# Optimization experiments

Measured on AMD Instinct MI355X. Metric: run time of the kernel, lower is better.

## Reference

```python
import jax, jax.numpy as jnp
import numpy as np

DIM = 1024
HEADS = 16
WIN = 128          # local window size
BATCH = 4
SEQ = 4096
HEAD_DIM = DIM // HEADS
HIDDEN = 2 * DIM   # GEGLU hidden_dim = 2*dim
EPS = 1e-5
NEG_INF = -1e9


def layer_norm(x, g, b):
    m = jnp.mean(x, axis=-1, keepdims=True)
    v = jnp.mean((x - m) ** 2, axis=-1, keepdims=True)
    return (x - m) * jax.lax.rsqrt(v + EPS) * g + b


def sliding_causal_local_attn(x, wq, wk, wv, wo, bo, rel_bias):
    # x: [B, S, D]; sliding-window causal attention: each query attends to
    # its own window plus the previous window (look_backward=1), causally masked.
    B, S, D = x.shape
    h, w, dh = HEADS, WIN, HEAD_DIM
    nw = S // w
    scale = dh ** -0.5

    def split_heads(t):  # [B,S,D] -> [B,h,nw,w,dh]
        return t.reshape(B, S, h, dh).transpose(0, 2, 1, 3).reshape(B, h, nw, w, dh)

    q = split_heads(x @ wq)
    k = split_heads(x @ wk)
    v = split_heads(x @ wv)

    # context = [previous window ; current window] -> [B,h,nw,2w,dh]
    k_pad = jnp.pad(k, ((0, 0), (0, 0), (1, 0), (0, 0), (0, 0)))
    v_pad = jnp.pad(v, ((0, 0), (0, 0), (1, 0), (0, 0), (0, 0)))
    kc = jnp.concatenate([k_pad[:, :, :-1], k_pad[:, :, 1:]], axis=3)
    vc = jnp.concatenate([v_pad[:, :, :-1], v_pad[:, :, 1:]], axis=3)

    logits = jnp.einsum('bhnid,bhnjd->bhnij', q, kc) * scale  # [B,h,nw,w,2w]

    i = jnp.arange(w)[:, None]        # query pos within window
    j = jnp.arange(2 * w)[None, :]    # key pos within [prev;cur] context
    dist = i + w - j                  # relative distance, 0..2w-1 when causal
    causal = dist >= 0
    # learned relative position bias per head, indexed by distance
    bias = rel_bias[:, jnp.clip(dist, 0, 2 * w - 1)]  # [h, w, 2w]
    logits = logits + bias[None, :, None]

    n_idx = jnp.arange(nw)[:, None, None]
    valid = causal[None] & ((n_idx > 0) | (j[None] >= w))  # mask padded first window
    logits = jnp.where(valid[None, None], logits, NEG_INF)

    attn = jax.nn.softmax(logits, axis=-1)
    out = jnp.einsum('bhnij,bhnjd->bhnid', attn, vc)           # [B,h,nw,w,dh]
    out = out.reshape(B, h, S, dh).transpose(0, 2, 1, 3).reshape(B, S, D)
    return out @ wo + bo


def geglu(x, w1, b1, w2, b2):
    proj = x @ w1 + b1                         # [B,S,2*HIDDEN]
    val, gate = jnp.split(proj, 2, axis=-1)
    return (val * jax.nn.gelu(gate, approximate=False)) @ w2 + b2


def setup_inputs() -> dict:
    key = jax.random.key(0)
    ks = jax.random.split(key, 12)
    sd = 0.02
    return {
        'x': jax.random.normal(ks[0], (BATCH, SEQ, DIM), jnp.float32),
        'ln1_g': jnp.ones((DIM,), jnp.float32),
        'ln1_b': jnp.zeros((DIM,), jnp.float32),
        'ln2_g': jnp.ones((DIM,), jnp.float32),
        'ln2_b': jnp.zeros((DIM,), jnp.float32),
        'wq': jax.random.normal(ks[1], (DIM, DIM), jnp.float32) * sd,
        'wk': jax.random.normal(ks[2], (DIM, DIM), jnp.float32) * sd,
        'wv': jax.random.normal(ks[3], (DIM, DIM), jnp.float32) * sd,
        'wo': jax.random.normal(ks[4], (DIM, DIM), jnp.float32) * sd,
        'bo': jnp.zeros((DIM,), jnp.float32),
        'rel_bias': jax.random.normal(ks[5], (HEADS, 2 * WIN), jnp.float32) * sd,
        'w_ff1': jax.random.normal(ks[6], (DIM, 2 * HIDDEN), jnp.float32) * sd,
        'b_ff1': jnp.zeros((2 * HIDDEN,), jnp.float32),
        'w_ff2': jax.random.normal(ks[7], (HIDDEN, DIM), jnp.float32) * sd,
        'b_ff2': jnp.zeros((DIM,), jnp.float32),
    }


def reference(x, ln1_g, ln1_b, ln2_g, ln2_b, wq, wk, wv, wo, bo, rel_bias,
              w_ff1, b_ff1, w_ff2, b_ff2):
    x = x + sliding_causal_local_attn(layer_norm(x, ln1_g, ln1_b),
                                      wq, wk, wv, wo, bo, rel_bias)
    x = x + geglu(layer_norm(x, ln2_g, ln2_b), w_ff1, b_ff1, w_ff2, b_ff2)
    return x
```

## Files before the change

kernel.cpp:

```cpp
#include <hip/hip_runtime.h>
#include <math.h>

typedef __attribute__((ext_vector_type(8))) short s16x8;
typedef __attribute__((ext_vector_type(4))) float f32x4;

__device__ __forceinline__ float b2f(unsigned short u){
  unsigned int i = ((unsigned int)u) << 16;
  float f; __builtin_memcpy(&f, &i, 4); return f;
}
__device__ __forceinline__ unsigned short f2b(float f){
  unsigned int i; __builtin_memcpy(&i, &f, 4);
  unsigned int r = (i + 0x7fffu + ((i >> 16) & 1u)) >> 16;
  return (unsigned short)r;
}
__device__ __forceinline__ f32x4 mfma16(s16x8 a, s16x8 b, f32x4 c){
  return __builtin_amdgcn_mfma_f32_16x16x32_bf16(a, b, c, 0, 0, 0);
}
__device__ __forceinline__ float gelu_exact(float x){
  return 0.5f * x * (1.0f + erff(x * 0.70710678118654752f));
}
__device__ __forceinline__ void gl_lds16(const unsigned short* g, unsigned short* l){
  __builtin_amdgcn_global_load_lds(
      (const __attribute__((address_space(1))) unsigned int*)g,
      (__attribute__((address_space(3))) unsigned int*)l, 16, 0, 0);
}

__global__ void transpose_k(const float* __restrict__ in,
                            unsigned short* __restrict__ out, int R, int C){
  __shared__ unsigned short tile[32][33];
  int c0 = blockIdx.x * 32, r0 = blockIdx.y * 32;
  int tx = threadIdx.x, ty = threadIdx.y;
  #pragma unroll
  for(int i = 0; i < 4; i++)
    tile[ty + 8*i][tx] = f2b(in[(size_t)(r0 + ty + 8*i) * C + c0 + tx]);
  __syncthreads();
  #pragma unroll
  for(int i = 0; i < 4; i++)
    out[(size_t)(c0 + ty + 8*i) * R + r0 + tx] = tile[tx][ty + 8*i];
}

__global__ __launch_bounds__(256) void ln_k(const float* __restrict__ x,
                                            const float* __restrict__ g,
                                            const float* __restrict__ b,
                                            unsigned short* __restrict__ out){
  int row = blockIdx.x, t = threadIdx.x;
  const float4* xr = (const float4*)(x + (size_t)row * 1024);
  float4 u = xr[t];
  float s  = u.x + u.y + u.z + u.w;
  float ss = u.x*u.x + u.y*u.y + u.z*u.z + u.w*u.w;
  for(int o = 32; o; o >>= 1){ s += __shfl_down(s, o, 64); ss += __shfl_down(ss, o, 64); }
  __shared__ float red[16];
  int lane = t & 63, wv = t >> 6;
  if(!lane){ red[wv] = s; red[8 + wv] = ss; }
  __syncthreads();
  if(!t){
    float S  = red[0] + red[1] + red[2] + red[3];
    float SS = red[8] + red[9] + red[10] + red[11];
    float m  = S * (1.0f/1024.0f);
    float var = SS * (1.0f/1024.0f) - m*m;
    red[0] = m; red[1] = rsqrtf(var + 1e-5f);
  }
  __syncthreads();
  float m = red[0], inv = red[1];
  float4 ug = ((const float4*)g)[t];
  float4 ub = ((const float4*)b)[t];
  ushort4 o4;
  o4.x = f2b((u.x - m) * inv * ug.x + ub.x);
  o4.y = f2b((u.y - m) * inv * ug.y + ub.y);
  o4.z = f2b((u.z - m) * inv * ug.z + ub.z);
  o4.w = f2b((u.w - m) * inv * ug.w + ub.w);
  ((ushort4*)(out + (size_t)row * 1024))[t] = o4;
}

__global__ __launch_bounds__(256) void gemm_bt(
    const unsigned short* __restrict__ A, const unsigned short* __restrict__ Bt,
    void* Cv, void* Cv2, int N, int n_split, int K,
    const float* __restrict__ bias, const float* res,
    const unsigned short* mul, int act_gelu, int c_fp32)
{
  __shared__ __align__(16) unsigned short As[128 * 64];
  __shared__ __align__(16) unsigned short Bs[128 * 64];

  int m_tile, n_tile;
  {
    unsigned int lin = blockIdx.y * gridDim.x + blockIdx.x;
    unsigned int mt = gridDim.y;
    if((mt & 7u) == 0u){
      unsigned int xcd = lin & 7u, idx = lin >> 3, mpx = mt >> 3;
      m_tile = xcd * mpx + (idx % mpx);
      n_tile = idx / mpx;
    } else { m_tile = blockIdx.y; n_tile = blockIdx.x; }
  }
  const int m0 = m_tile * 128, n0 = n_tile * 128;
  const int tid = threadIdx.x;
  const int wave = tid >> 6, lane = tid & 63;
  const int wm = (wave >> 1) * 64, wn = (wave & 1) * 64;
  const int lrow = lane & 15, quad = lane >> 4;

  const int tr  = tid >> 3;
  const int scg = ((tid & 7) ^ (tr & 7)) * 8;
  const int xw  = lrow & 7;

  f32x4 acc[4][4];
  #pragma unroll
  for(int i = 0; i < 4; i++)
    #pragma unroll
    for(int j = 0; j < 4; j++)
      #pragma unroll
      for(int r = 0; r < 4; r++) acc[i][j][r] = 0.0f;

  const int nk = K >> 6;
  for(int kt = 0; kt < nk; kt++){
    const int k0 = kt << 6;
    if(kt) __syncthreads();
    #pragma unroll
    for(int i = 0; i < 4; i++){
      int row = i*32 + tr;
      gl_lds16(&A [(size_t)(m0 + row)*K + k0 + scg], &As[i*2048 + wave*512]);
      gl_lds16(&Bt[(size_t)(n0 + row)*K + k0 + scg], &Bs[i*2048 + wave*512]);
    }
    __syncthreads();
    #pragma unroll
    for(int kk = 0; kk < 2; kk++){
      s16x8 af[4], bfv[4];
      #pragma unroll
      for(int i = 0; i < 4; i++){
        int ga = ((kk<<2) + quad) ^ xw;
        af [i] = *(const s16x8*)&As[(wm + i*16 + lrow)*64 + ga*8];
        bfv[i] = *(const s16x8*)&Bs[(wn + i*16 + lrow)*64 + ga*8];
      }
      #pragma unroll
      for(int i = 0; i < 4; i++)
        #pragma unroll
        for(int j = 0; j < 4; j++)
          acc[i][j] = mfma16(af[i], bfv[j], acc[i][j]);
    }
  }
  const int qr = quad * 4;
  #pragma unroll
  for(int i = 0; i < 4; i++){
    #pragma unroll
    for(int j = 0; j < 4; j++){
      int col = n0 + wn + j*16 + lrow;
      float bv = bias ? bias[col] : 0.0f;
      #pragma unroll
      for(int r = 0; r < 4; r++){
        int row = m0 + wm + i*16 + qr + r;
        float v = acc[i][j][r] + bv;
        if(act_gelu) v = gelu_exact(v);
        if(col < n_split){
          size_t idx = (size_t)row * n_split + col;
          if(mul) v *= b2f(mul[idx]);
          if(res) v += res[idx];
          if(c_fp32) ((float*)Cv)[idx] = v;
          else       ((unsigned short*)Cv)[idx] = f2b(v);
        } else {
          size_t idx = (size_t)row * (N - n_split) + (col - n_split);
          ((unsigned short*)Cv2)[idx] = f2b(v);
        }
      }
    }
  }
}

__global__ __launch_bounds__(256, 1) void attn_k(const unsigned short* __restrict__ qk,
                                                 const unsigned short* __restrict__ vbuf,
                                                 const float* __restrict__ rel_bias,
                                                 unsigned short* __restrict__ attn_out)
{
  __shared__ unsigned short kvS[128 * 72];
  __shared__ unsigned short PS[128 * 136];
  __shared__ float biasS[256];

  const int n = blockIdx.x, h = blockIdx.y, b = blockIdx.z;
  const int tid = threadIdx.x;
  const int wave = tid >> 6, lane = tid & 63;
  const int lrow = lane & 15, quad = lane >> 4, lk = quad * 8;
  const int rbase = wave * 32;
  const size_t rowbase = (size_t)b * 4096;
  const int prev = (n > 0) ? (n - 1) : 0;

  biasS[tid] = rel_bias[h * 256 + tid];

  s16x8 aq[2][2];
  #pragma unroll
  for(int mi = 0; mi < 2; mi++)
    #pragma unroll
    for(int kk = 0; kk < 2; kk++)
      aq[mi][kk] = *(const s16x8*)&qk[(rowbase + n*128 + rbase + mi*16 + lrow)*2048
                                      + h*64 + kk*32 + lk];

  f32x4 lg[2][16];
  #pragma unroll
  for(int mi = 0; mi < 2; mi++)
    #pragma unroll
    for(int nj = 0; nj < 16; nj++)
      #pragma unroll
      for(int r = 0; r < 4; r++) lg[mi][nj][r] = 0.0f;

  for(int jh = 0; jh < 2; jh++){
    if(jh) __syncthreads();
    #pragma unroll
    for(int it = 0; it < 4; it++){
      int cid = tid + it * 256;
      int jloc = cid >> 3, c8 = (cid & 7) * 8;
      int j = jh * 128 + jloc;
      int srow = (j < 128) ? (prev*128 + j) : (n*128 + j - 128);
      *(s16x8*)&kvS[jloc*72 + c8] =
        *(const s16x8*)&qk[(rowbase + srow)*2048 + 1024 + h*64 + c8];
    }
    __syncthreads();
    #pragma unroll
    for(int njl = 0; njl < 8; njl++){
      #pragma unroll
      for(int kk = 0; kk < 2; kk++){
        s16x8 bk = *(const s16x8*)&kvS[(njl*16 + lrow)*72 + kk*32 + lk];
        #pragma unroll
        for(int mi = 0; mi < 2; mi++)
          lg[mi][jh*8 + njl] = mfma16(aq[mi][kk], bk, lg[mi][jh*8 + njl]);
      }
    }
  }
  __syncthreads();

  #pragma unroll
  for(int mi = 0; mi < 2; mi++){
    #pragma unroll
    for(int r = 0; r < 4; r++){
      int i = rbase + mi*16 + quad*4 + r;
      float mx = -3e38f;
      #pragma unroll
      for(int nj = 0; nj < 16; nj++){
        int j = nj*16 + lrow;
        int dist = i + 128 - j;
        bool valid = (dist >= 0) && ((n > 0) || (j >= 128));
        float l = valid ? (lg[mi][nj][r] * 0.125f + biasS[dist & 255]) : -1e9f;
        lg[mi][nj][r] = l;
        mx = fmaxf(mx, l);
      }
      #pragma unroll
      for(int o = 1; o < 16; o <<= 1) mx = fmaxf(mx, __shfl_xor(mx, o, 64));
      float s = 0.0f;
      #pragma unroll
      for(int nj = 0; nj < 16; nj++){
        float p = __expf(lg[mi][nj][r] - mx);
        lg[mi][nj][r] = p;
        s += p;
      }
      #pragma unroll
      for(int o = 1; o < 16; o <<= 1) s += __shfl_xor(s, o, 64);
      float inv = 1.0f / s;
      #pragma unroll
      for(int nj = 0; nj < 16; nj++) lg[mi][nj][r] *= inv;
    }
  }

  f32x4 o_acc[2][4];
  #pragma unroll
  for(int mi = 0; mi < 2; mi++)
    #pragma unroll
    for(int nj = 0; nj < 4; nj++)
      #pragma unroll
      for(int r = 0; r < 4; r++) o_acc[mi][nj][r] = 0.0f;

  for(int jh = 0; jh < 2; jh++){
    {
      int jloc = tid >> 1;
      int dbase = (tid & 1) * 32;
      int j = jh * 128 + jloc;
      int srow = (j < 128) ? (prev*128 + j) : (n*128 + j - 128);
      const unsigned short* vr = &vbuf[(rowbase + srow)*1024 + h*64 + dbase];
      #pragma unroll
      for(int i8 = 0; i8 < 4; i8++){
        s16x8 vv = *(const s16x8*)&vr[i8 * 8];
        #pragma unroll
        for(int e = 0; e < 8; e++)
          kvS[(dbase + i8*8 + e)*136 + jloc] = (unsigned short)vv[e];
      }
    }
    #pragma unroll
    for(int mi = 0; mi < 2; mi++)
      #pragma unroll
      for(int r = 0; r < 4; r++)
        #pragma unroll
        for(int njl = 0; njl < 8; njl++)
          PS[(rbase + mi*16 + quad*4 + r)*136 + njl*16 + lrow] = f2b(lg[mi][jh*8 + njl][r]);
    __syncthreads();
    #pragma unroll
    for(int kk = 0; kk < 4; kk++){
      s16x8 ap[2];
      #pragma unroll
      for(int mi = 0; mi < 2; mi++)
        ap[mi] = *(const s16x8*)&PS[(rbase + mi*16 + lrow)*136 + kk*32 + lk];
      #pragma unroll
      for(int nj = 0; nj < 4; nj++){
        s16x8 bv = *(const s16x8*)&kvS[(nj*16 + lrow)*136 + kk*32 + lk];
        #pragma unroll
        for(int mi = 0; mi < 2; mi++)
          o_acc[mi][nj] = mfma16(ap[mi], bv, o_acc[mi][nj]);
      }
    }
    __syncthreads();
  }

  #pragma unroll
  for(int mi = 0; mi < 2; mi++)
    #pragma unroll
    for(int nj = 0; nj < 4; nj++)
      #pragma unroll
      for(int r = 0; r < 4; r++){
        size_t row = rowbase + n*128 + rbase + mi*16 + quad*4 + r;
        int col = h*64 + nj*16 + lrow;
        attn_out[row * 1024 + col] = f2b(o_acc[mi][nj][r]);
      }
}

extern "C" void kernel_launch(void* const* d_in, const int* in_sizes, int n_in,
                              void* d_out, int out_size, void* d_ws, size_t ws_size,
                              hipStream_t stream) {
  const float* x     = (const float*)d_in[0];
  const float* ln1_g = (const float*)d_in[1];
  const float* ln1_b = (const float*)d_in[2];
  const float* ln2_g = (const float*)d_in[3];
  const float* ln2_b = (const float*)d_in[4];
  const float* wq    = (const float*)d_in[5];
  const float* wk    = (const float*)d_in[6];
  const float* wv    = (const float*)d_in[7];
  const float* wo    = (const float*)d_in[8];
  const float* bo    = (const float*)d_in[9];
  const float* rel   = (const float*)d_in[10];
  const float* wff1  = (const float*)d_in[11];
  const float* bff1  = (const float*)d_in[12];
  const float* wff2  = (const float*)d_in[13];
  const float* bff2  = (const float*)d_in[14];
  float* out = (float*)d_out;
  char*  ws  = (char*)d_ws;

  unsigned short* wqkvT = (unsigned short*)(ws);
  unsigned short* woT   = (unsigned short*)(ws +  6291456);
  unsigned short* wff1T = (unsigned short*)(ws +  8388608);
  unsigned short* wff2T = (unsigned short*)(ws + 16777216);
  unsigned short* h     = (unsigned short*)(ws + 20971520);
  unsigned short* qk    = (unsigned short*)(ws + 54525952);
  unsigned short* ff    = qk;
  unsigned short* vbuf  = (unsigned short*)d_out;
  float*          x1    = out;

  dim3 tb(32, 8);
  transpose_k<<<dim3(32, 32),  tb, 0, stream>>>(wq,   wqkvT,           1024, 1024);
  transpose_k<<<dim3(32, 32),  tb, 0, stream>>>(wk,   wqkvT + 1048576, 1024, 1024);
  transpose_k<<<dim3(32, 32),  tb, 0, stream>>>(wv,   wqkvT + 2097152, 1024, 1024);
  transpose_k<<<dim3(32, 32),  tb, 0, stream>>>(wo,   woT,             1024, 1024);
  transpose_k<<<dim3(128, 32), tb, 0, stream>>>(wff1, wff1T,           1024, 4096);
  transpose_k<<<dim3(32, 64),  tb, 0, stream>>>(wff2, wff2T,           2048, 1024);

  ln_k<<<16384, 256, 0, stream>>>(x, ln1_g, ln1_b, h);
  gemm_bt<<<dim3(24, 128), 256, 0, stream>>>(h, wqkvT, qk, vbuf, 3072, 2048, 1024,
                                             nullptr, nullptr, nullptr, 0, 0);
  attn_k<<<dim3(32, 16, 4), 256, 0, stream>>>(qk, vbuf, rel, h);
  gemm_bt<<<dim3(8, 128), 256, 0, stream>>>(h, woT, x1, nullptr, 1024, 1024, 1024,
                                            bo, x, nullptr, 0, 1);
  ln_k<<<16384, 256, 0, stream>>>(x1, ln2_g, ln2_b, h);
  gemm_bt<<<dim3(16, 128), 256, 0, stream>>>(h, wff1T + 2048*1024, ff, nullptr, 2048, 2048, 1024,
                                             bff1 + 2048, nullptr, nullptr, 1, 0);
  gemm_bt<<<dim3(16, 128), 256, 0, stream>>>(h, wff1T, ff, nullptr, 2048, 2048, 1024,
                                             bff1, nullptr, ff, 0, 0);
  gemm_bt<<<dim3(8, 128), 256, 0, stream>>>(ff, wff2T, out, nullptr, 1024, 1024, 2048,
                                            bff2, x1, nullptr, 0, 1);
}
```

Measured before the change: 894.0 us.

## Fuse GEGLU value/gate GEMMs and merge weight transposes with first layernorm

```diff
diff --git a/kernel.cpp b/kernel.cpp
--- a/kernel.cpp
+++ b/kernel.cpp
@@ -25,11 +25,71 @@
       (__attribute__((address_space(3))) unsigned int*)l, 16, 0, 0);
 }
 
-__global__ void transpose_k(const float* __restrict__ in,
-                            unsigned short* __restrict__ out, int R, int C){
+__device__ __forceinline__ void ln_row(const float* __restrict__ xrow,
+                                       const float* __restrict__ g,
+                                       const float* __restrict__ b,
+                                       unsigned short* __restrict__ orow, int lane){
+  const float4* xr = (const float4*)xrow;
+  float4 u[4];
+  #pragma unroll
+  for(int q = 0; q < 4; q++) u[q] = xr[lane + 64*q];
+  float s = 0.0f, ss = 0.0f;
+  #pragma unroll
+  for(int q = 0; q < 4; q++){
+    s  += u[q].x + u[q].y + u[q].z + u[q].w;
+    ss += u[q].x*u[q].x + u[q].y*u[q].y + u[q].z*u[q].z + u[q].w*u[q].w;
+  }
+  #pragma unroll
+  for(int o = 32; o; o >>= 1){ s += __shfl_xor(s, o, 64); ss += __shfl_xor(ss, o, 64); }
+  float m = s * (1.0f/1024.0f);
+  float inv = rsqrtf(ss * (1.0f/1024.0f) - m*m + 1e-5f);
+  #pragma unroll
+  for(int q = 0; q < 4; q++){
+    float4 ug = ((const float4*)g)[lane + 64*q];
+    float4 ub = ((const float4*)b)[lane + 64*q];
+    ushort4 o4;
+    o4.x = f2b((u[q].x - m) * inv * ug.x + ub.x);
+    o4.y = f2b((u[q].y - m) * inv * ug.y + ub.y);
+    o4.z = f2b((u[q].z - m) * inv * ug.z + ub.z);
+    o4.w = f2b((u[q].w - m) * inv * ug.w + ub.w);
+    ((ushort4*)orow)[lane + 64*q] = o4;
+  }
+}
+
+__global__ __launch_bounds__(256) void prep_k(
+    const float* __restrict__ x, const float* __restrict__ ln1_g, const float* __restrict__ ln1_b,
+    unsigned short* __restrict__ h,
+    const float* __restrict__ wq, const float* __restrict__ wk, const float* __restrict__ wv,
+    const float* __restrict__ wo, const float* __restrict__ wff1, const float* __restrict__ wff2,
+    unsigned short* __restrict__ wqkvT, unsigned short* __restrict__ woT,
+    unsigned short* __restrict__ wff1T, unsigned short* __restrict__ wff2T)
+{
+  const int bz = blockIdx.x;
+  if(bz >= 10240){
+    int id = bz - 10240;
+    int lane = threadIdx.x & 63, wave = threadIdx.x >> 6;
+    int row = id * 4 + wave;
+    ln_row(x + (size_t)row*1024, ln1_g, ln1_b, h + (size_t)row*1024, lane);
+    return;
+  }
+  const float* in; unsigned short* out; int R, C, c0, r0;
+  if(bz < 4096){
+    int w = bz >> 10, id = bz & 1023;
+    const float* srcs[4] = {wq, wk, wv, wo};
+    unsigned short* dsts[4] = {wqkvT, wqkvT + 1048576, wqkvT + 2097152, woT};
+    in = srcs[w]; out = dsts[w]; R = 1024; C = 1024;
+    c0 = (id & 31) * 32; r0 = (id >> 5) * 32;
+  } else if(bz < 8192){
+    int id = bz - 4096;
+    in = wff1; out = wff1T; R = 1024; C = 4096;
+    c0 = (id & 127) * 32; r0 = (id >> 7) * 32;
+  } else {
+    int id = bz - 8192;
+    in = wff2; out = wff2T; R = 2048; C = 1024;
+    c0 = (id & 31) * 32; r0 = (id >> 5) * 32;
+  }
   __shared__ unsigned short tile[32][33];
-  int c0 = blockIdx.x * 32, r0 = blockIdx.y * 32;
-  int tx = threadIdx.x, ty = threadIdx.y;
+  int tx = threadIdx.x & 31, ty = threadIdx.x >> 5;
   #pragma unroll
   for(int i = 0; i < 4; i++)
     tile[ty + 8*i][tx] = f2b(in[(size_t)(r0 + ty + 8*i) * C + c0 + tx]);
@@ -39,44 +99,19 @@
     out[(size_t)(c0 + ty + 8*i) * R + r0 + tx] = tile[tx][ty + 8*i];
 }
 
-__global__ __launch_bounds__(256) void ln_k(const float* __restrict__ x,
-                                            const float* __restrict__ g,
-                                            const float* __restrict__ b,
-                                            unsigned short* __restrict__ out){
-  int row = blockIdx.x, t = threadIdx.x;
-  const float4* xr = (const float4*)(x + (size_t)row * 1024);
-  float4 u = xr[t];
-  float s  = u.x + u.y + u.z + u.w;
-  float ss = u.x*u.x + u.y*u.y + u.z*u.z + u.w*u.w;
-  for(int o = 32; o; o >>= 1){ s += __shfl_down(s, o, 64); ss += __shfl_down(ss, o, 64); }
-  __shared__ float red[16];
-  int lane = t & 63, wv = t >> 6;
-  if(!lane){ red[wv] = s; red[8 + wv] = ss; }
-  __syncthreads();
-  if(!t){
-    float S  = red[0] + red[1] + red[2] + red[3];
-    float SS = red[8] + red[9] + red[10] + red[11];
-    float m  = S * (1.0f/1024.0f);
-    float var = SS * (1.0f/1024.0f) - m*m;
-    red[0] = m; red[1] = rsqrtf(var + 1e-5f);
-  }
-  __syncthreads();
-  float m = red[0], inv = red[1];
-  float4 ug = ((const float4*)g)[t];
-  float4 ub = ((const float4*)b)[t];
-  ushort4 o4;
-  o4.x = f2b((u.x - m) * inv * ug.x + ub.x);
-  o4.y = f2b((u.y - m) * inv * ug.y + ub.y);
-  o4.z = f2b((u.z - m) * inv * ug.z + ub.z);
-  o4.w = f2b((u.w - m) * inv * ug.w + ub.w);
-  ((ushort4*)(out + (size_t)row * 1024))[t] = o4;
+__global__ __launch_bounds__(256) void ln2_k(const float* __restrict__ x,
+                                             const float* __restrict__ g,
+                                             const float* __restrict__ b,
+                                             unsigned short* __restrict__ out){
+  int lane = threadIdx.x & 63, wave = threadIdx.x >> 6;
+  int row = blockIdx.x * 4 + wave;
+  ln_row(x + (size_t)row*1024, g, b, out + (size_t)row*1024, lane);
 }
 
 __global__ __launch_bounds__(256) void gemm_bt(
     const unsigned short* __restrict__ A, const unsigned short* __restrict__ Bt,
     void* Cv, void* Cv2, int N, int n_split, int K,
-    const float* __restrict__ bias, const float* res,
-    const unsigned short* mul, int act_gelu, int c_fp32)
+    const float* __restrict__ bias, const float* res, int c_fp32)
 {
   __shared__ __align__(16) unsigned short As[128 * 64];
   __shared__ __align__(16) unsigned short Bs[128 * 64];
@@ -85,11 +120,9 @@
   {
     unsigned int lin = blockIdx.y * gridDim.x + blockIdx.x;
     unsigned int mt = gridDim.y;
-    if((mt & 7u) == 0u){
-      unsigned int xcd = lin & 7u, idx = lin >> 3, mpx = mt >> 3;
-      m_tile = xcd * mpx + (idx % mpx);
-      n_tile = idx / mpx;
-    } else { m_tile = blockIdx.y; n_tile = blockIdx.x; }
+    unsigned int xcd = lin & 7u, idx = lin >> 3, mpx = mt >> 3;
+    m_tile = xcd * mpx + (idx % mpx);
+    n_tile = idx / mpx;
   }
   const int m0 = m_tile * 128, n0 = n_tile * 128;
   const int tid = threadIdx.x;
@@ -147,10 +180,8 @@
       for(int r = 0; r < 4; r++){
         int row = m0 + wm + i*16 + qr + r;
         float v = acc[i][j][r] + bv;
-        if(act_gelu) v = gelu_exact(v);
         if(col < n_split){
           size_t idx = (size_t)row * n_split + col;
-          if(mul) v *= b2f(mul[idx]);
           if(res) v += res[idx];
           if(c_fp32) ((float*)Cv)[idx] = v;
           else       ((unsigned short*)Cv)[idx] = f2b(v);
@@ -160,6 +191,102 @@
         }
       }
     }
+  }
+}
+
+__global__ __launch_bounds__(256) void geglu_gemm(
+    const unsigned short* __restrict__ A, const unsigned short* __restrict__ Bt,
+    unsigned short* __restrict__ C, int K,
+    const float* __restrict__ bias)
+{
+  __shared__ __align__(16) unsigned short pool[2 * 128 * 64];
+  unsigned short* As = pool;
+  unsigned short* Bs = pool + 128*64;
+
+  int m_tile, n_tile;
+  {
+    unsigned int lin = blockIdx.y * gridDim.x + blockIdx.x;
+    unsigned int mt = gridDim.y;
+    unsigned int xcd = lin & 7u, idx = lin >> 3, mpx = mt >> 3;
+    m_tile = xcd * mpx + (idx % mpx);
+    n_tile = idx / mpx;
+  }
+  const int m0 = m_tile * 128, nv0 = n_tile * 64;
+  const int tid = threadIdx.x;
+  const int wave = tid >> 6, lane = tid & 63;
+  const int wm = (wave >> 1) * 64, wn = (wave & 1) * 64;
+  const int lrow = lane & 15, quad = lane >> 4;
+
+  const int tr  = tid >> 3;
+  const int scg = ((tid & 7) ^ (tr & 7)) * 8;
+  const int xw  = lrow & 7;
+
+  f32x4 acc[4][4];
+  #pragma unroll
+  for(int i = 0; i < 4; i++)
+    #pragma unroll
+    for(int j = 0; j < 4; j++)
+      #pragma unroll
+      for(int r = 0; r < 4; r++) acc[i][j][r] = 0.0f;
+
+  const int nk = K >> 6;
+  for(int kt = 0; kt < nk; kt++){
+    const int k0 = kt << 6;
+    if(kt) __syncthreads();
+    #pragma unroll
+    for(int i = 0; i < 4; i++){
+      int row = i*32 + tr;
+      int brow = (row < 64) ? (nv0 + row) : (2048 + nv0 + row - 64);
+      gl_lds16(&A [(size_t)(m0 + row)*K + k0 + scg], &As[i*2048 + wave*512]);
+      gl_lds16(&Bt[(size_t)brow     *K + k0 + scg], &Bs[i*2048 + wave*512]);
+    }
+    __syncthreads();
+    #pragma unroll
+    for(int kk = 0; kk < 2; kk++){
+      s16x8 af[4], bfv[4];
+      #pragma unroll
+      for(int i = 0; i < 4; i++){
+        int ga = ((kk<<2) + quad) ^ xw;
+        af [i] = *(const s16x8*)&As[(wm + i*16 + lrow)*64 + ga*8];
+        bfv[i] = *(const s16x8*)&Bs[(wn + i*16 + lrow)*64 + ga*8];
+      }
+      #pragma unroll
+      for(int i = 0; i < 4; i++)
+        #pragma unroll
+        for(int j = 0; j < 4; j++)
+          acc[i][j] = mfma16(af[i], bfv[j], acc[i][j]);
+    }
+  }
+  __syncthreads();
+  float* gS = (float*)pool;
+  const int qr = quad * 4;
+  if(wn == 64){
+    #pragma unroll
+    for(int i = 0; i < 4; i++)
+      #pragma unroll
+      for(int j = 0; j < 4; j++){
+        int cl = j*16 + lrow;
+        float bv = bias[2048 + nv0 + cl];
+        #pragma unroll
+        for(int r = 0; r < 4; r++)
+          gS[(wm + i*16 + qr + r)*64 + cl] = gelu_exact(acc[i][j][r] + bv);
+      }
+  }
+  __syncthreads();
+  if(wn == 0){
+    #pragma unroll
+    for(int i = 0; i < 4; i++)
+      #pragma unroll
+      for(int j = 0; j < 4; j++){
+        int cl = j*16 + lrow;
+        float bv = bias[nv0 + cl];
+        #pragma unroll
+        for(int r = 0; r < 4; r++){
+          int rl = wm + i*16 + qr + r;
+          float v = (acc[i][j][r] + bv) * gS[rl*64 + cl];
+          C[(size_t)(m0 + rl) * 2048 + nv0 + cl] = f2b(v);
+        }
+      }
   }
 }
 
@@ -346,25 +473,16 @@
   unsigned short* vbuf  = (unsigned short*)d_out;
   float*          x1    = out;
 
-  dim3 tb(32, 8);
-  transpose_k<<<dim3(32, 32),  tb, 0, stream>>>(wq,   wqkvT,           1024, 1024);
-  transpose_k<<<dim3(32, 32),  tb, 0, stream>>>(wk,   wqkvT + 1048576, 1024, 1024);
-  transpose_k<<<dim3(32, 32),  tb, 0, stream>>>(wv,   wqkvT + 2097152, 1024, 1024);
-  transpose_k<<<dim3(32, 32),  tb, 0, stream>>>(wo,   woT,             1024, 1024);
-  transpose_k<<<dim3(128, 32), tb, 0, stream>>>(wff1, wff1T,           1024, 4096);
-  transpose_k<<<dim3(32, 64),  tb, 0, stream>>>(wff2, wff2T,           2048, 1024);
-
-  ln_k<<<16384, 256, 0, stream>>>(x, ln1_g, ln1_b, h);
+  prep_k<<<14336, 256, 0, stream>>>(x, ln1_g, ln1_b, h,
+                                    wq, wk, wv, wo, wff1, wff2,
+                                    wqkvT, woT, wff1T, wff2T);
   gemm_bt<<<dim3(24, 128), 256, 0, stream>>>(h, wqkvT, qk, vbuf, 3072, 2048, 1024,
-                                             nullptr, nullptr, nullptr, 0, 0);
+                                             nullptr, nullptr, 0);
   attn_k<<<dim3(32, 16, 4), 256, 0, stream>>>(qk, vbuf, rel, h);
   gemm_bt<<<dim3(8, 128), 256, 0, stream>>>(h, woT, x1, nullptr, 1024, 1024, 1024,
-                                            bo, x, nullptr, 0, 1);
-  ln_k<<<16384, 256, 0, stream>>>(x1, ln2_g, ln2_b, h);
-  gemm_bt<<<dim3(16, 128), 256, 0, stream>>>(h, wff1T + 2048*1024, ff, nullptr, 2048, 2048, 1024,
-                                             bff1 + 2048, nullptr, nullptr, 1, 0);
-  gemm_bt<<<dim3(16, 128), 256, 0, stream>>>(h, wff1T, ff, nullptr, 2048, 2048, 1024,
-                                             bff1, nullptr, ff, 0, 0);
+                                            bo, x, 1);
+  ln2_k<<<4096, 256, 0, stream>>>(x1, ln2_g, ln2_b, h);
+  geglu_gemm<<<dim3(32, 128), 256, 0, stream>>>(h, wff1T, ff, 1024, bff1);
   gemm_bt<<<dim3(8, 128), 256, 0, stream>>>(ff, wff2T, out, nullptr, 1024, 1024, 2048,
-                                            bff2, x1, nullptr, 0, 1);
-}
+                                            bff2, x1, 1);
+}
```

Result: faster. 796.1 us (-10.9%).
